# Optimization experiments

Hardware: AMD Instinct MI355X
Metric: run time of the kernel (lower is better)

Reference implementation:

```python
import jax, jax.numpy as jnp
import numpy as np

N = 64
EPS = 1e-4
N_ITER = 100
BRANCH = 10


def setup_inputs() -> dict:
    key = jax.random.key(0)
    x = jax.random.normal(key, (8192, 4096), dtype=jnp.float32)
    return {"x": x}


def _lml(x):
    # x: [n_batch, nx], nx > N assumed (as configured in setup_inputs)
    n_batch, nx = x.shape
    x_sorted = jnp.sort(x, axis=1)[:, ::-1]  # descending
    nu_lower = -x_sorted[:, N - 1] - 7.0  # [n_batch]
    nu_upper = -x_sorted[:, N] + 7.0      # [n_batch]
    ls = jnp.linspace(0.0, 1.0, BRANCH).astype(x.dtype)  # [branch]
    rows = jnp.arange(n_batch)

    def cond(state):
        i, lo, hi = state
        return (i < N_ITER) & jnp.any(hi - lo > EPS)

    def body(state):
        i, lo, hi = state
        r = hi - lo                     # [n_batch]
        I = r > EPS                     # rows still being refined
        nus = r[:, None] * ls + lo[:, None]  # [n_batch, branch]
        # sigmoid-sum constraint at each candidate nu: [n_batch, branch]
        fs = jax.nn.sigmoid(x[:, None, :] + nus[:, :, None]).sum(axis=2) - N
        neg = (fs < 0).sum(axis=1) - 1  # index of last negative iterate
        J = neg < 0                     # all-positive-iterates warning case
        i_lower = jnp.clip(neg, 0, BRANCH - 2)
        new_lo = nus[rows, i_lower]
        new_hi = nus[rows, i_lower + 1]
        new_lo = jnp.where(J, new_lo - 7.0, new_lo)
        lo = jnp.where(I, new_lo, lo)
        hi = jnp.where(I, new_hi, hi)
        return i + 1, lo, hi

    _, lo, hi = jax.lax.while_loop(cond, body, (0, nu_lower, nu_upper))
    nu = lo + (hi - lo) / 2.0
    return jax.nn.sigmoid(x + nu[:, None])


def reference(x):
    return _lml(x)
```

## Files before the change

kernel.cpp:

```cpp
#include <hip/hip_runtime.h>

#define ROWLEN 4096
#define TPB    256
#define PER    16
#define NTARGET 64.0f
#define LOG2E  1.44269504088896340736f

#if __has_builtin(__builtin_amdgcn_exp2f)
__device__ __forceinline__ float exp2_fast(float x) { return __builtin_amdgcn_exp2f(x); }
#else
__device__ __forceinline__ float exp2_fast(float x) {
    float r; asm("v_exp_f32 %0, %1" : "=v"(r) : "v"(x)); return r;
}
#endif

#if __has_builtin(__builtin_amdgcn_rcpf)
__device__ __forceinline__ float rcp_fast(float x) { return __builtin_amdgcn_rcpf(x); }
#else
__device__ __forceinline__ float rcp_fast(float x) {
    float r; asm("v_rcp_f32 %0, %1" : "=v"(r) : "v"(x)); return r;
}
#endif

__device__ __forceinline__ float sig_from(float v, float tnu) {
    float e = exp2_fast(fmaf(v, -LOG2E, tnu));
    return rcp_fast(1.0f + e);
}

__global__ __launch_bounds__(TPB) void lml_kernel(const float* __restrict__ x,
                                                  float* __restrict__ out) {
    const int t = threadIdx.x;
    const size_t base = (size_t)blockIdx.x * ROWLEN;

    float v[PER];
#pragma unroll
    for (int k = 0; k < 4; ++k) {
        float4 f = reinterpret_cast<const float4*>(x + base)[t + k * TPB];
        v[4*k+0] = f.x; v[4*k+1] = f.y; v[4*k+2] = f.z; v[4*k+3] = f.w;
    }

    __shared__ float lds[8];
    const int wave = t >> 6;

    float mx = v[0], mn = v[0];
#pragma unroll
    for (int i = 1; i < PER; ++i) { mx = fmaxf(mx, v[i]); mn = fminf(mn, v[i]); }
#pragma unroll
    for (int off = 32; off >= 1; off >>= 1) {
        mx = fmaxf(mx, __shfl_xor(mx, off, 64));
        mn = fminf(mn, __shfl_xor(mn, off, 64));
    }
    if ((t & 63) == 0) { lds[wave] = mx; lds[4 + wave] = mn; }
    __syncthreads();
    mx = fmaxf(fmaxf(lds[0], lds[1]), fmaxf(lds[2], lds[3]));
    mn = fminf(fminf(lds[4], lds[5]), fminf(lds[6], lds[7]));
    __syncthreads();

    float lo = -mx - 7.0f;
    float hi = -mn;
    float nu;

#pragma unroll 1
    for (int it = 0; it < 10; ++it) {
        nu = 0.5f * (lo + hi);
        const float tnu = -LOG2E * nu;
        float s = 0.0f;
#pragma unroll
        for (int i = 0; i < PER; ++i) s += sig_from(v[i], tnu);
#pragma unroll
        for (int off = 32; off >= 1; off >>= 1) s += __shfl_xor(s, off, 64);
        if ((t & 63) == 0) lds[wave] = s;
        __syncthreads();
        const float fs = (lds[0] + lds[1]) + (lds[2] + lds[3]) - NTARGET;
        __syncthreads();
        if (fs < 0.0f) lo = nu; else hi = nu;
    }

    nu = 0.5f * (lo + hi);
#pragma unroll 1
    for (int it = 0; it < 3; ++it) {
        const float tnu = -LOG2E * nu;
        float s = 0.0f, w = 0.0f;
#pragma unroll
        for (int i = 0; i < PER; ++i) {
            const float si = sig_from(v[i], tnu);
            s += si;
            w = fmaf(si, -si, w + si);
        }
#pragma unroll
        for (int off = 32; off >= 1; off >>= 1) {
            s += __shfl_xor(s, off, 64);
            w += __shfl_xor(w, off, 64);
        }
        if ((t & 63) == 0) { lds[wave] = s; lds[4 + wave] = w; }
        __syncthreads();
        const float fs = (lds[0] + lds[1]) + (lds[2] + lds[3]) - NTARGET;
        const float fw = (lds[4] + lds[5]) + (lds[6] + lds[7]);
        __syncthreads();
        if (fs < 0.0f) lo = nu; else hi = nu;
        float nun = nu - fs / fmaxf(fw, 1e-12f);
        if (!(nun > lo && nun < hi)) nun = 0.5f * (lo + hi);
        nu = nun;
    }

    const float tnu = -LOG2E * nu;
#pragma unroll
    for (int k = 0; k < 4; ++k) {
        float4 f;
        f.x = sig_from(v[4*k+0], tnu);
        f.y = sig_from(v[4*k+1], tnu);
        f.z = sig_from(v[4*k+2], tnu);
        f.w = sig_from(v[4*k+3], tnu);
        reinterpret_cast<float4*>(out + base)[t + k * TPB] = f;
    }
}

extern "C" void kernel_launch(void* const* d_in, const int* in_sizes, int n_in,
                              void* d_out, int out_size, void* d_ws, size_t ws_size,
                              hipStream_t stream) {
    const float* x = (const float*)d_in[0];
    float* out = (float*)d_out;
    const int rows = in_sizes[0] / ROWLEN;
    lml_kernel<<<rows, TPB, 0, stream>>>(x, out);
}
```

Baseline: 267.7 us.

## Replace bisection with log-sum-exp initial guess and log-space Newton steps

Drops the 10-iteration bisection loop and seeds nu from an analytic lower bound, nu = ln(64) - ln(sum exp(x)). Since sigmoid(z) <= exp(z), the sigmoid sum at that nu is at most 64, so it brackets the root with hi = -min(x). The three Newton iterations now solve log(sum sigmoid) = log(64), which converges faster from the low side. This removes ten full passes of exp/rcp plus their block reductions and barriers, but relies on three log-space Newton steps from the new guess being accurate enough, and exp(x) without max-subtraction can overflow for large inputs.

Result: faster. 227.7 us (-14.9%).

```diff
diff --git a/kernel.cpp b/kernel.cpp
--- a/kernel.cpp
+++ b/kernel.cpp
@@ -6,21 +6,15 @@
 #define NTARGET 64.0f
 #define LOG2E  1.44269504088896340736f
 
-#if __has_builtin(__builtin_amdgcn_exp2f)
-__device__ __forceinline__ float exp2_fast(float x) { return __builtin_amdgcn_exp2f(x); }
-#else
 __device__ __forceinline__ float exp2_fast(float x) {
     float r; asm("v_exp_f32 %0, %1" : "=v"(r) : "v"(x)); return r;
 }
-#endif
-
-#if __has_builtin(__builtin_amdgcn_rcpf)
-__device__ __forceinline__ float rcp_fast(float x) { return __builtin_amdgcn_rcpf(x); }
-#else
 __device__ __forceinline__ float rcp_fast(float x) {
     float r; asm("v_rcp_f32 %0, %1" : "=v"(r) : "v"(x)); return r;
 }
-#endif
+__device__ __forceinline__ float log2_fast(float x) {
+    float r; asm("v_log_f32 %0, %1" : "=v"(r) : "v"(x)); return r;
+}
 
 __device__ __forceinline__ float sig_from(float v, float tnu) {
     float e = exp2_fast(fmaf(v, -LOG2E, tnu));
@@ -39,44 +33,30 @@
         v[4*k+0] = f.x; v[4*k+1] = f.y; v[4*k+2] = f.z; v[4*k+3] = f.w;
     }
 
+    float S = 0.0f, mn = v[0];
+#pragma unroll
+    for (int i = 0; i < PER; ++i) {
+        S += exp2_fast(v[i] * LOG2E);
+        mn = fminf(mn, v[i]);
+    }
+
     __shared__ float lds[8];
     const int wave = t >> 6;
-
-    float mx = v[0], mn = v[0];
-#pragma unroll
-    for (int i = 1; i < PER; ++i) { mx = fmaxf(mx, v[i]); mn = fminf(mn, v[i]); }
 #pragma unroll
     for (int off = 32; off >= 1; off >>= 1) {
-        mx = fmaxf(mx, __shfl_xor(mx, off, 64));
+        S += __shfl_xor(S, off, 64);
         mn = fminf(mn, __shfl_xor(mn, off, 64));
     }
-    if ((t & 63) == 0) { lds[wave] = mx; lds[4 + wave] = mn; }
+    if ((t & 63) == 0) { lds[wave] = S; lds[4 + wave] = mn; }
     __syncthreads();
-    mx = fmaxf(fmaxf(lds[0], lds[1]), fmaxf(lds[2], lds[3]));
+    S  = (lds[0] + lds[1]) + (lds[2] + lds[3]);
     mn = fminf(fminf(lds[4], lds[5]), fminf(lds[6], lds[7]));
     __syncthreads();
 
-    float lo = -mx - 7.0f;
+    float nu = (6.0f - log2_fast(S)) * (1.0f / LOG2E);
+    float lo = nu;
     float hi = -mn;
-    float nu;
 
-#pragma unroll 1
-    for (int it = 0; it < 10; ++it) {
-        nu = 0.5f * (lo + hi);
-        const float tnu = -LOG2E * nu;
-        float s = 0.0f;
-#pragma unroll
-        for (int i = 0; i < PER; ++i) s += sig_from(v[i], tnu);
-#pragma unroll
-        for (int off = 32; off >= 1; off >>= 1) s += __shfl_xor(s, off, 64);
-        if ((t & 63) == 0) lds[wave] = s;
-        __syncthreads();
-        const float fs = (lds[0] + lds[1]) + (lds[2] + lds[3]) - NTARGET;
-        __syncthreads();
-        if (fs < 0.0f) lo = nu; else hi = nu;
-    }
-
-    nu = 0.5f * (lo + hi);
 #pragma unroll 1
     for (int it = 0; it < 3; ++it) {
         const float tnu = -LOG2E * nu;
@@ -94,11 +74,12 @@
         }
         if ((t & 63) == 0) { lds[wave] = s; lds[4 + wave] = w; }
         __syncthreads();
-        const float fs = (lds[0] + lds[1]) + (lds[2] + lds[3]) - NTARGET;
+        const float fs = (lds[0] + lds[1]) + (lds[2] + lds[3]);
         const float fw = (lds[4] + lds[5]) + (lds[6] + lds[7]);
         __syncthreads();
-        if (fs < 0.0f) lo = nu; else hi = nu;
-        float nun = nu - fs / fmaxf(fw, 1e-12f);
+        if (fs < NTARGET) lo = nu; else hi = nu;
+        const float h = (log2_fast(fs) - 6.0f) * (1.0f / LOG2E);
+        float nun = nu - h * fs * rcp_fast(fmaxf(fw, 1e-20f));
         if (!(nun > lo && nun < hi)) nun = 0.5f * (lo + hi);
         nu = nun;
     }
```
